# Performance work log

Hardware: AMD Instinct MI355X
Metric: run time of the kernel (lower is better)

Reference implementation:

```python
import jax, jax.numpy as jnp
import numpy as np

DIM = 2048
N_HEADS = 32
HEAD_DIM = DIM // N_HEADS  # 64
ROT_DIM = 32               # partial_rotary_factor = 32/head_dim
ROPE_THETA = 1000000.0
T = 2048
QKV_DIM = 3 * DIM


def setup_inputs() -> dict:
    key = jax.random.key(0)
    ks = jax.random.split(key, 8)
    inp = {
        "positions": jnp.arange(T, dtype=jnp.int32),
        "hidden_states": jax.random.normal(ks[0], (T, DIM), dtype=jnp.float32),
        "Wqkv": jax.random.normal(ks[1], (QKV_DIM, DIM), dtype=jnp.float32) * 0.02,
        "bqkv": jax.random.normal(ks[2], (QKV_DIM,), dtype=jnp.float32) * 0.02,
        "Wout": jax.random.normal(ks[3], (DIM, DIM), dtype=jnp.float32) * 0.02,
        "bout": jax.random.normal(ks[4], (DIM,), dtype=jnp.float32) * 0.02,
        "tau_alpha": jax.random.normal(ks[5], (N_HEADS,), dtype=jnp.float32) * 0.1,
        "tau_wq": jax.random.normal(ks[6], (N_HEADS, QKV_DIM), dtype=jnp.float32) * 0.02,
        "tau_wv": jax.random.normal(ks[7], (N_HEADS, QKV_DIM), dtype=jnp.float32) * 0.02,
    }
    return inp


def _rope_neox(x, positions):
    # x: [T, H, D]; rotate first ROT_DIM dims, neox (half-split) style
    half = ROT_DIM // 2
    inv_freq = 1.0 / (ROPE_THETA ** (jnp.arange(0, ROT_DIM, 2, dtype=jnp.float32) / ROT_DIM))
    ang = positions.astype(jnp.float32)[:, None] * inv_freq[None, :]  # [T, half]
    cos = jnp.cos(ang)[:, None, :]  # [T, 1, half]
    sin = jnp.sin(ang)[:, None, :]
    x1 = x[..., :half]
    x2 = x[..., half:ROT_DIM]
    rot = jnp.concatenate([x1 * cos - x2 * sin, x2 * cos + x1 * sin], axis=-1)
    return jnp.concatenate([rot, x[..., ROT_DIM:]], axis=-1)


def reference(positions, hidden_states, Wqkv, bqkv, Wout, bout, tau_alpha, tau_wq, tau_wv):
    T_, H, D = hidden_states.shape[0], N_HEADS, HEAD_DIM
    qkv = hidden_states @ Wqkv.T + bqkv  # [T, 3*DIM]
    q, k, v = jnp.split(qkv, [DIM, 2 * DIM], axis=-1)

    # tau gating (exact-erf gelu, matching torch F.gelu default)
    tok_feat = jax.nn.gelu(qkv, approximate=False)
    tok_q = jnp.tanh(tok_feat @ tau_wq.T)  # [T, H]
    tok_v = jnp.tanh(tok_feat @ tau_wv.T)
    pos_log = jnp.log(jnp.clip(positions.astype(jnp.float32) + 1.0, 1e-6))  # [T]
    tau_pos = 1.0 + (jax.nn.sigmoid(tau_alpha[None, :] * pos_log[:, None]) - 0.5)  # [T, H]
    tau_q = tok_q + tau_pos
    tau_v = tok_v + tau_pos

    q = q.reshape(T_, H, D) * tau_q[:, :, None]
    k = k.reshape(T_, H, D)
    v = v.reshape(T_, H, D) * tau_v[:, :, None]

    q = _rope_neox(q, positions)
    k = _rope_neox(k, positions)

    # causal attention
    scale = D ** -0.5
    scores = jnp.einsum("thd,shd->hts", q, k) * scale  # [H, T, T]
    causal = positions[:, None] >= positions[None, :]   # [T, T]
    scores = jnp.where(causal[None, :, :], scores, jnp.finfo(scores.dtype).min)
    probs = jax.nn.softmax(scores, axis=-1)
    attn = jnp.einsum("hts,shd->thd", probs, v).reshape(T_, DIM)

    return attn @ Wout.T + bout
```

## Files before the change

kernel.cpp:

```cpp
#include <hip/hip_runtime.h>
#include <math.h>


typedef __bf16 bf16x8 __attribute__((ext_vector_type(8)));
typedef float floatx4 __attribute__((ext_vector_type(4)));
typedef unsigned short ushort8v __attribute__((ext_vector_type(8)));

__device__ __forceinline__ unsigned short f2b(float x) {
    unsigned int b = __float_as_uint(x);
    b = b + 0x7FFFu + ((b >> 16) & 1u);
    return (unsigned short)(b >> 16);
}
__device__ __forceinline__ unsigned short f2b_trunc(float x) {
    return (unsigned short)(__float_as_uint(x) >> 16);
}
__device__ __forceinline__ float b2f(unsigned short u) {
    return __uint_as_float(((unsigned int)u) << 16);
}
__device__ __forceinline__ float gelu_f(float x) {
    return 0.5f * x * (1.0f + erff(x * 0.70710678118654752440f));
}
__device__ __forceinline__ float fexp2(float x) {
    return __builtin_amdgcn_exp2f(x);
}
__device__ __forceinline__ floatx4 mfma16(bf16x8 a, bf16x8 b, floatx4 c) {
    return __builtin_amdgcn_mfma_f32_16x16x32_bf16(a, b, c, 0, 0, 0);
}
__device__ __forceinline__ void gl2lds16(const unsigned short* g, unsigned short* l) {
    __builtin_amdgcn_global_load_lds(
        (__attribute__((address_space(1))) void*)g,
        (__attribute__((address_space(3))) void*)l, 16, 0, 0);
}

__constant__ float INV_FREQ[16] = {
    1.0f, 0.42169650342858224f, 0.17782794100389228f, 0.074989420933245582f,
    0.031622776601683791f, 0.013335214321633240f, 0.0056234132519034908f,
    0.0023713737056616552f, 0.001f, 4.2169650342858224e-4f,
    1.7782794100389228e-4f, 7.4989420933245582e-5f, 3.1622776601683791e-5f,
    1.3335214321633240e-5f, 5.6234132519034908e-6f, 2.3713737056616552e-6f
};

__constant__ unsigned char CHUNK_QT[40] = {
    15,15,15, 14,14,14, 13,13,13, 12,12,12, 11,11, 10,10, 9,9, 8,8, 7,6,5,4,
    15,11,7,3, 14,10,6,2, 13,9,5,1, 12,8,4,0};
__constant__ unsigned char CHUNK_C[40] = {
    0,1,2, 0,1,2, 0,1,2, 0,1,2, 0,1, 0,1, 0,1, 0,1, 0,0,0,0,
    3,2,1,0, 3,2,1,0, 3,2,1,0, 3,2,1,0};

__global__ __launch_bounds__(256) void cvt3_f32_bf16(
    const float* __restrict__ s0, unsigned short* __restrict__ d0, int n0,
    const float* __restrict__ s1, unsigned short* __restrict__ d1, int n1,
    const float* __restrict__ s2, unsigned short* __restrict__ d2, int n2) {
    int i = blockIdx.x * 256 + threadIdx.x;
    const float* s; unsigned short* d;
    if (i < n0)           { s = s0; d = d0; }
    else if (i < n0 + n1) { i -= n0; s = s1; d = d1; }
    else                  { i -= n0 + n1; s = s2; d = d2; if (i >= n2) return; }
    const float4* sp = reinterpret_cast<const float4*>(s) + (size_t)i * 2;
    float4 a = sp[0], b = sp[1];
    ushort8v r;
    r[0] = f2b(a.x); r[1] = f2b(a.y); r[2] = f2b(a.z); r[3] = f2b(a.w);
    r[4] = f2b(b.x); r[5] = f2b(b.y); r[6] = f2b(b.z); r[7] = f2b(b.w);
    *(reinterpret_cast<ushort8v*>(d) + i) = r;
}

__global__ __launch_bounds__(256, 2) void gemm_qkv_p2(
    const unsigned short* __restrict__ A, const unsigned short* __restrict__ B,
    const float* __restrict__ bias, unsigned short* __restrict__ P,
    int M, int N, int K) {
    __shared__ unsigned short Ls[2][20480];
    const int tid = threadIdx.x;
    const int wave = tid >> 6, lane = tid & 63;
    const int row16 = lane & 15, quad = lane >> 4;
    const int wrow = wave >> 1, wcol = wave & 1;
    const int bm0 = blockIdx.y * 128, bn0 = blockIdx.x * 192;
    const int NT = K >> 6;

    floatx4 acc[4][6] = {};

    auto stage_half = [&](int kt, int hf) {
        const bool isB = hf & 1;
        const unsigned short* mat = isB ? B : A;
        const int rbase = isB ? bn0 : bm0;
        const int colb = kt * 64 + (hf >> 1) * 32;
        const int hoff = ((hf & 1) ? 4096 : 0) + (hf >> 1) * 10240;
        unsigned short* dst = &Ls[kt & 1][hoff];
        const int nrd = isB ? 3 : 2;
        #pragma unroll
        for (int rd = 0; rd < 3; ++rd) {
            if (rd >= nrd) break;
            int g = tid + rd * 256;
            int rl = g & 7, c4 = (g >> 3) & 3, r8 = g >> 5;
            gl2lds16(mat + (size_t)(rbase + r8 * 8 + rl) * K + colb + c4 * 8,
                     dst + g * 8);
        }
    };

    stage_half(0, 0); stage_half(0, 1); stage_half(0, 2); stage_half(0, 3);
    stage_half(1, 0); stage_half(1, 1); stage_half(1, 2);
    asm volatile("s_waitcnt vmcnt(7)" ::: "memory");
    __builtin_amdgcn_s_barrier();

    const int ra = wrow * 64 + row16;
    const int rb = wcol * 96 + row16;
    const int aoff = (ra >> 3) * 256 + quad * 64 + (ra & 7) * 8;
    const int boff = (rb >> 3) * 256 + quad * 64 + (rb & 7) * 8;

    for (int kt = 0; kt < NT; ++kt) {
        const int bsel = kt & 1;
        bf16x8 af[4], bfr[3];
        #pragma unroll
        for (int mt = 0; mt < 4; ++mt)
            af[mt] = *reinterpret_cast<const bf16x8*>(&Ls[bsel][aoff + mt * 512]);
        #pragma unroll
        for (int j = 0; j < 3; ++j)
            bfr[j] = *reinterpret_cast<const bf16x8*>(&Ls[bsel][4096 + boff + j * 512]);
        if (kt + 1 < NT) stage_half(kt + 1, 3);
        __builtin_amdgcn_s_barrier();
        asm volatile("s_waitcnt lgkmcnt(0)" ::: "memory");
        __builtin_amdgcn_sched_barrier(0);
        __builtin_amdgcn_s_setprio(1);
        #pragma unroll
        for (int mt = 0; mt < 4; ++mt)
            #pragma unroll
            for (int j = 0; j < 3; ++j)
                acc[mt][j] = mfma16(af[mt], bfr[j], acc[mt][j]);
        __builtin_amdgcn_s_setprio(0);
        __builtin_amdgcn_s_barrier();
        #pragma unroll
        for (int j = 0; j < 3; ++j)
            bfr[j] = *reinterpret_cast<const bf16x8*>(&Ls[bsel][4096 + boff + (3 + j) * 512]);
        if (kt + 2 < NT) stage_half(kt + 2, 0);
        __builtin_amdgcn_s_barrier();
        asm volatile("s_waitcnt lgkmcnt(0)" ::: "memory");
        __builtin_amdgcn_sched_barrier(0);
        __builtin_amdgcn_s_setprio(1);
        #pragma unroll
        for (int mt = 0; mt < 4; ++mt)
            #pragma unroll
            for (int j = 0; j < 3; ++j)
                acc[mt][3 + j] = mfma16(af[mt], bfr[j], acc[mt][3 + j]);
        __builtin_amdgcn_s_setprio(0);
        __builtin_amdgcn_s_barrier();
        #pragma unroll
        for (int mt = 0; mt < 4; ++mt)
            af[mt] = *reinterpret_cast<const bf16x8*>(&Ls[bsel][10240 + aoff + mt * 512]);
        #pragma unroll
        for (int j = 0; j < 3; ++j)
            bfr[j] = *reinterpret_cast<const bf16x8*>(&Ls[bsel][14336 + boff + j * 512]);
        if (kt + 2 < NT) stage_half(kt + 2, 1);
        __builtin_amdgcn_s_barrier();
        asm volatile("s_waitcnt lgkmcnt(0)" ::: "memory");
        __builtin_amdgcn_sched_barrier(0);
        __builtin_amdgcn_s_setprio(1);
        #pragma unroll
        for (int mt = 0; mt < 4; ++mt)
            #pragma unroll
            for (int j = 0; j < 3; ++j)
                acc[mt][j] = mfma16(af[mt], bfr[j], acc[mt][j]);
        __builtin_amdgcn_s_setprio(0);
        __builtin_amdgcn_s_barrier();
        #pragma unroll
        for (int j = 0; j < 3; ++j)
            bfr[j] = *reinterpret_cast<const bf16x8*>(&Ls[bsel][14336 + boff + (3 + j) * 512]);
        if (kt + 2 < NT) stage_half(kt + 2, 2);
        if (kt == NT - 2)     asm volatile("s_waitcnt vmcnt(0)" ::: "memory");
        else if (kt < NT - 2) asm volatile("s_waitcnt vmcnt(7)" ::: "memory");
        __builtin_amdgcn_s_barrier();
        asm volatile("s_waitcnt lgkmcnt(0)" ::: "memory");
        __builtin_amdgcn_sched_barrier(0);
        __builtin_amdgcn_s_setprio(1);
        #pragma unroll
        for (int mt = 0; mt < 4; ++mt)
            #pragma unroll
            for (int j = 0; j < 3; ++j)
                acc[mt][3 + j] = mfma16(af[mt], bfr[j], acc[mt][3 + j]);
        __builtin_amdgcn_s_setprio(0);
        __builtin_amdgcn_s_barrier();
    }

    #pragma unroll
    for (int mt = 0; mt < 4; ++mt) {
        #pragma unroll
        for (int nt = 0; nt < 6; ++nt) {
            int gc = bn0 + wcol * 96 + nt * 16 + row16;
            float bv = bias[gc];
            int gr0 = bm0 + wrow * 64 + mt * 16 + quad * 4;
            #pragma unroll
            for (int i = 0; i < 4; ++i)
                P[(size_t)(gr0 + i) * N + gc] = f2b(acc[mt][nt][i] + bv);
        }
    }
}

template <int BM, int BN, bool OUT_BF16>
__global__ __launch_bounds__(256) void gemm_bf16_bt(
    const unsigned short* __restrict__ A, const unsigned short* __restrict__ B,
    const float* __restrict__ bias, void* __restrict__ Cout,
    int M, int N, int K) {
    constexpr int MT = BM / 32, NT = BN / 32;
    __shared__ unsigned short As[BM * 64];
    __shared__ unsigned short Bs[BN * 64];
    const int tid = threadIdx.x;
    const int wave = tid >> 6, lane = tid & 63;
    const int row16 = lane & 15, quad = lane >> 4;
    const int wm = (wave >> 1) * (BM / 2), wn = (wave & 1) * (BN / 2);
    const int bm0 = blockIdx.y * BM, bn0 = blockIdx.x * BN;
    const int rl = lane & 7, cl = lane >> 3;

    floatx4 acc[MT][NT] = {};

    for (int k0 = 0; k0 < K; k0 += 64) {
        __syncthreads();
        #pragma unroll
        for (int j = 0; j < BM / 32; ++j) {
            int unit = wave * (BM / 32) + j;
            const unsigned short* ga = A + (size_t)(bm0 + unit * 8 + rl) * K + k0 + cl * 8;
            gl2lds16(ga, &As[unit * 512 + lane * 8]);
        }
        #pragma unroll
        for (int j = 0; j < BN / 32; ++j) {
            int unit = wave * (BN / 32) + j;
            const unsigned short* gb = B + (size_t)(bn0 + unit * 8 + rl) * K + k0 + cl * 8;
            gl2lds16(gb, &Bs[unit * 512 + lane * 8]);
        }
        __syncthreads();

        #pragma unroll
        for (int ks = 0; ks < 2; ++ks) {
            bf16x8 af[MT], bfr[NT];
            #pragma unroll
            for (int mt = 0; mt < MT; ++mt) {
                int r = wm + mt * 16 + row16;
                af[mt] = *reinterpret_cast<const bf16x8*>(
                    &As[(r >> 3) * 512 + (ks * 4 + quad) * 64 + (r & 7) * 8]);
            }
            #pragma unroll
            for (int nt = 0; nt < NT; ++nt) {
                int r = wn + nt * 16 + row16;
                bfr[nt] = *reinterpret_cast<const bf16x8*>(
                    &Bs[(r >> 3) * 512 + (ks * 4 + quad) * 64 + (r & 7) * 8]);
            }
            #pragma unroll
            for (int mt = 0; mt < MT; ++mt)
                #pragma unroll
                for (int nt = 0; nt < NT; ++nt)
                    acc[mt][nt] = mfma16(af[mt], bfr[nt], acc[mt][nt]);
        }
    }

    #pragma unroll
    for (int mt = 0; mt < MT; ++mt) {
        #pragma unroll
        for (int nt = 0; nt < NT; ++nt) {
            int gc = bn0 + wn + nt * 16 + row16;
            float bv = bias[gc];
            int gr0 = bm0 + wm + mt * 16 + quad * 4;
            #pragma unroll
            for (int i = 0; i < 4; ++i) {
                float v = acc[mt][nt][i] + bv;
                if (OUT_BF16)
                    ((unsigned short*)Cout)[(size_t)(gr0 + i) * N + gc] = f2b(v);
                else
                    ((float*)Cout)[(size_t)(gr0 + i) * N + gc] = v;
            }
        }
    }
}

template <int KSPLIT>
__global__ __launch_bounds__(256) void tok_gemm_splitk(
    const unsigned short* __restrict__ A0,
    const float* __restrict__ Bq, const float* __restrict__ Bv,
    float* __restrict__ C, int K) {
    constexpr int LDT = 72;
    __shared__ unsigned short As[64 * LDT];
    __shared__ unsigned short Bs[64 * LDT];
    const int tid = threadIdx.x;
    const int wave = tid >> 6, lane = tid & 63;
    const int row16 = lane & 15, quad = lane >> 4;
    const int wm = (wave >> 1) * 32, wn = (wave & 1) * 32;
    const int bm0 = blockIdx.y * 64;
    const int kbeg = blockIdx.x * KSPLIT;

    floatx4 acc[2][2] = {};

    for (int k0 = kbeg; k0 < kbeg + KSPLIT; k0 += 64) {
        #pragma unroll
        for (int it = 0; it < 2; ++it) {
            int i = tid + it * 256;
            int r = i >> 3, c8 = i & 7;
            size_t off = (size_t)(bm0 + r) * K + k0 + c8 * 8;
            ushort8v a0 = *reinterpret_cast<const ushort8v*>(A0 + off);
            ushort8v g;
            #pragma unroll
            for (int j = 0; j < 8; ++j) g[j] = f2b(gelu_f(b2f(a0[j])));
            *reinterpret_cast<ushort8v*>(&As[r * LDT + c8 * 8]) = g;

            const float* brow = (r < 32) ? (Bq + (size_t)r * K) : (Bv + (size_t)(r - 32) * K);
            float4 w0 = *reinterpret_cast<const float4*>(brow + k0 + c8 * 8);
            float4 w1 = *reinterpret_cast<const float4*>(brow + k0 + c8 * 8 + 4);
            ushort8v wb;
            wb[0] = f2b(w0.x); wb[1] = f2b(w0.y); wb[2] = f2b(w0.z); wb[3] = f2b(w0.w);
            wb[4] = f2b(w1.x); wb[5] = f2b(w1.y); wb[6] = f2b(w1.z); wb[7] = f2b(w1.w);
            *reinterpret_cast<ushort8v*>(&Bs[r * LDT + c8 * 8]) = wb;
        }
        __syncthreads();

        #pragma unroll
        for (int ks = 0; ks < 2; ++ks) {
            bf16x8 af[2], bfr[2];
            #pragma unroll
            for (int mt = 0; mt < 2; ++mt)
                af[mt] = *reinterpret_cast<const bf16x8*>(
                    &As[(wm + mt * 16 + row16) * LDT + ks * 32 + quad * 8]);
            #pragma unroll
            for (int nt = 0; nt < 2; ++nt)
                bfr[nt] = *reinterpret_cast<const bf16x8*>(
                    &Bs[(wn + nt * 16 + row16) * LDT + ks * 32 + quad * 8]);
            #pragma unroll
            for (int mt = 0; mt < 2; ++mt)
                #pragma unroll
                for (int nt = 0; nt < 2; ++nt)
                    acc[mt][nt] = mfma16(af[mt], bfr[nt], acc[mt][nt]);
        }
        __syncthreads();
    }

    #pragma unroll
    for (int mt = 0; mt < 2; ++mt)
        #pragma unroll
        for (int nt = 0; nt < 2; ++nt) {
            int gc = wn + nt * 16 + row16;
            int gr0 = bm0 + wm + mt * 16 + quad * 4;
            #pragma unroll
            for (int i = 0; i < 4; ++i)
                atomicAdd(&C[(size_t)(gr0 + i) * 64 + gc], acc[mt][nt][i]);
        }
}

__global__ __launch_bounds__(256) void qkv_process(
    const unsigned short* __restrict__ P,
    const float* __restrict__ tok_raw, const float* __restrict__ tau_alpha,
    const int* __restrict__ positions, unsigned short* __restrict__ qh,
    unsigned short* __restrict__ kh, unsigned short* __restrict__ vpk) {
    const int h = blockIdx.y;
    const int t0 = blockIdx.x * 64;
    const int tid = threadIdx.x;
    __shared__ float vtr[64][65];
    __shared__ float tauq_s[64], tauv_s[64];

    if (tid < 64) {
        int t = t0 + tid;
        float pos = (float)positions[t];
        float pl = logf(fmaxf(pos + 1.0f, 1e-6f));
        float a = tau_alpha[h];
        float tp = 0.5f + 1.0f / (1.0f + __expf(-a * pl));
        tauq_s[tid] = tanhf(tok_raw[t * 64 + h]) + tp;
        tauv_s[tid] = tanhf(tok_raw[t * 64 + 32 + h]) + tp;
    }
    __syncthreads();

    const float QSCALE = 0.18033688011112042f;
    #pragma unroll
    for (int it = 0; it < 2; ++it) {
        int idx = tid + it * 256;
        int tl = idx >> 3, c8 = idx & 7;
        int t = t0 + tl;
        size_t rb = (size_t)t * 6144 + h * 64 + c8 * 8;
        ushort8v q0v = *reinterpret_cast<const ushort8v*>(P + rb);
        ushort8v k0v = *reinterpret_cast<const ushort8v*>(P + rb + 2048);
        ushort8v v0v = *reinterpret_cast<const ushort8v*>(P + rb + 4096);
        float tq = tauq_s[tl], tv = tauv_s[tl];
        float qo[8], ko[8];
        #pragma unroll
        for (int j = 0; j < 8; ++j) {
            qo[j] = b2f(q0v[j]) * tq;
            ko[j] = b2f(k0v[j]);
        }
        if (c8 < 4) {
            size_t rp = (size_t)t * 6144 + h * 64 + (c8 ^ 2) * 8;
            ushort8v qp0 = *reinterpret_cast<const ushort8v*>(P + rp);
            ushort8v kp0 = *reinterpret_cast<const ushort8v*>(P + rp + 2048);
            float pos = (float)positions[t];
            float sgn = (c8 < 2) ? -1.0f : 1.0f;
            #pragma unroll
            for (int j = 0; j < 8; ++j) {
                int fi = (c8 * 8 + j) & 15;
                float ang = pos * INV_FREQ[fi];
                float s, c;
                sincosf(ang, &s, &c);
                float qp = b2f(qp0[j]) * tq;
                float kp = b2f(kp0[j]);
                qo[j] = qo[j] * c + sgn * qp * s;
                ko[j] = ko[j] * c + sgn * kp * s;
            }
        }
        size_t ob = ((size_t)h * 2048 + t) * 64 + c8 * 8;
        ushort8v qw, kw;
        #pragma unroll
        for (int j = 0; j < 8; ++j) {
            qw[j] = f2b(qo[j] * QSCALE);
            kw[j] = f2b(ko[j]);
        }
        *reinterpret_cast<ushort8v*>(qh + ob) = qw;
        *reinterpret_cast<ushort8v*>(kh + ob) = kw;
        #pragma unroll
        for (int j = 0; j < 8; ++j)
            vtr[c8 * 8 + j][tl] = b2f(v0v[j]) * tv;
    }
    __syncthreads();
    #pragma unroll
    for (int it = 0; it < 2; ++it) {
        int idx = tid + it * 256;
        int d = idx >> 3, tc = (idx & 7) * 8;
        int sb = (t0 + tc) >> 5;
        int quad = (tc & 31) >> 3;
        int nt = d >> 4, m = d & 15;
        ushort8v w;
        #pragma unroll
        for (int j = 0; j < 8; ++j) w[j] = f2b(vtr[d][tc + j]);
        *reinterpret_cast<ushort8v*>(
            vpk + (size_t)h * 131072 + sb * 2048 + nt * 512 + quad * 128 + m * 8) = w;
    }
}

__global__ __launch_bounds__(256) void attn_fa(
    const unsigned short* __restrict__ qh, const unsigned short* __restrict__ kh,
    const unsigned short* __restrict__ vpk, unsigned short* __restrict__ Opart,
    float* __restrict__ ml) {
    constexpr int LD = 72;
    __shared__ unsigned short pbuf[4][2][16 * LD];
    const int b = blockIdx.x;
    const int h = (b & 7) + 8 * ((b >> 3) & 3);
    const int cpos = b >> 5;
    const int qt = CHUNK_QT[cpos], ch = CHUNK_C[cpos];
    const int q0 = qt * 128;
    const int slot = (h * 16 + qt) * 4 + ch;
    const int wave = threadIdx.x >> 6, lane = threadIdx.x & 63;
    const int m = lane & 15, quad = lane >> 4;
    const int qrow0 = q0 + wave * 32;
    const int sbeg = ch * 512;
    const int send = min(sbeg + 512, qrow0 + 32);

    bf16x8 aq[2][2];
    #pragma unroll
    for (int mt = 0; mt < 2; ++mt) {
        const unsigned short* qptr = qh + ((size_t)h * 2048 + qrow0 + mt * 16 + m) * 64;
        aq[mt][0] = *reinterpret_cast<const bf16x8*>(qptr + quad * 8);
        aq[mt][1] = *reinterpret_cast<const bf16x8*>(qptr + 32 + quad * 8);
    }
    const unsigned short* kbase = kh + (size_t)h * 2048 * 64;
    const unsigned short* vbase = vpk + (size_t)h * 131072;

    floatx4 o[2][4] = {};
    float lsum[2][4] = {};

    for (int s0 = sbeg; s0 < send; s0 += 64) {
        floatx4 sc[2][4];
        #pragma unroll
        for (int sg = 0; sg < 4; ++sg) {
            const unsigned short* kr = kbase + (size_t)(s0 + sg * 16 + m) * 64;
            bf16x8 bk0 = *reinterpret_cast<const bf16x8*>(kr + quad * 8);
            bf16x8 bk1 = *reinterpret_cast<const bf16x8*>(kr + 32 + quad * 8);
            #pragma unroll
            for (int mt = 0; mt < 2; ++mt) {
                floatx4 z = {};
                z = mfma16(aq[mt][0], bk0, z);
                z = mfma16(aq[mt][1], bk1, z);
                sc[mt][sg] = z;
            }
        }
        if (s0 + 63 > qrow0) {
            #pragma unroll
            for (int mt = 0; mt < 2; ++mt)
                #pragma unroll
                for (int sg = 0; sg < 4; ++sg)
                    #pragma unroll
                    for (int i = 0; i < 4; ++i) {
                        int t = qrow0 + mt * 16 + quad * 4 + i;
                        int s = s0 + sg * 16 + m;
                        sc[mt][sg][i] = (s > t) ? -1e30f : sc[mt][sg][i];
                    }
        }
        #pragma unroll
        for (int mt = 0; mt < 2; ++mt)
            #pragma unroll
            for (int sg = 0; sg < 4; ++sg)
                #pragma unroll
                for (int i = 0; i < 4; ++i)
                    sc[mt][sg][i] = fexp2(sc[mt][sg][i]);
        #pragma unroll
        for (int mt = 0; mt < 2; ++mt)
            #pragma unroll
            for (int i = 0; i < 4; ++i)
                lsum[mt][i] += (sc[mt][0][i] + sc[mt][1][i]) + (sc[mt][2][i] + sc[mt][3][i]);

        unsigned short* pb0 = pbuf[wave][0];
        unsigned short* pb1 = pbuf[wave][1];
        #pragma unroll
        for (int sg = 0; sg < 4; ++sg)
            #pragma unroll
            for (int i = 0; i < 4; ++i) {
                pb0[(quad * 4 + i) * LD + sg * 16 + m] = f2b_trunc(sc[0][sg][i]);
                pb1[(quad * 4 + i) * LD + sg * 16 + m] = f2b_trunc(sc[1][sg][i]);
            }
        bf16x8 ap[2][2];
        #pragma unroll
        for (int mt = 0; mt < 2; ++mt) {
            ap[mt][0] = *reinterpret_cast<const bf16x8*>(&pbuf[wave][mt][m * LD + quad * 8]);
            ap[mt][1] = *reinterpret_cast<const bf16x8*>(&pbuf[wave][mt][m * LD + 32 + quad * 8]);
        }
        #pragma unroll
        for (int c = 0; c < 2; ++c) {
            const unsigned short* vrow = vbase + ((s0 >> 5) + c) * 2048;
            #pragma unroll
            for (int nt = 0; nt < 4; ++nt) {
                bf16x8 bv = *reinterpret_cast<const bf16x8*>(vrow + nt * 512 + lane * 8);
                o[0][nt] = mfma16(ap[0][c], bv, o[0][nt]);
                o[1][nt] = mfma16(ap[1][c], bv, o[1][nt]);
            }
        }
    }

    #pragma unroll
    for (int d = 1; d < 16; d <<= 1)
        #pragma unroll
        for (int mt = 0; mt < 2; ++mt)
            #pragma unroll
            for (int i = 0; i < 4; ++i)
                lsum[mt][i] += __shfl_xor(lsum[mt][i], d, 16);
    #pragma unroll
    for (int mt = 0; mt < 2; ++mt) {
        #pragma unroll
        for (int nt = 0; nt < 4; ++nt)
            #pragma unroll
            for (int i = 0; i < 4; ++i)
                Opart[((size_t)slot * 128 + wave * 32 + mt * 16 + quad * 4 + i) * 64 + nt * 16 + m]
                    = f2b(o[mt][nt][i]);
        if (m == 0) {
            #pragma unroll
            for (int i = 0; i < 4; ++i)
                ml[(size_t)slot * 128 + wave * 32 + mt * 16 + quad * 4 + i] = lsum[mt][i];
        }
    }
}

__global__ __launch_bounds__(256) void attn_merge(
    const unsigned short* __restrict__ Opart, const float* __restrict__ ml,
    unsigned short* __restrict__ attnb) {
    const int qt = blockIdx.x, h = blockIdx.y;
    const int nc = qt / 4 + 1;
    const int tid = threadIdx.x;
    const int r = tid >> 1, dh = (tid & 1) * 32;
    const int bs = (h * 16 + qt) * 4;

    float denom = 0.0f;
    #pragma unroll
    for (int c = 0; c < 4; ++c)
        if (c < nc) denom += ml[(size_t)(bs + c) * 128 + r];
    float inv = 1.0f / denom;

    float acc[32] = {};
    #pragma unroll
    for (int c = 0; c < 4; ++c) {
        if (c < nc) {
            const unsigned short* op = Opart + ((size_t)(bs + c) * 128 + r) * 64 + dh;
            #pragma unroll
            for (int j = 0; j < 4; ++j) {
                ushort8v v = *reinterpret_cast<const ushort8v*>(op + j * 8);
                #pragma unroll
                for (int k = 0; k < 8; ++k)
                    acc[j * 8 + k] += b2f(v[k]);
            }
        }
    }
    unsigned short* dst = attnb + (size_t)(qt * 128 + r) * 2048 + h * 64 + dh;
    #pragma unroll
    for (int j = 0; j < 4; ++j) {
        ushort8v v;
        #pragma unroll
        for (int k = 0; k < 8; ++k) v[k] = f2b(acc[j * 8 + k] * inv);
        *reinterpret_cast<ushort8v*>(dst + j * 8) = v;
    }
}

extern "C" void kernel_launch(void* const* d_in, const int* in_sizes, int n_in,
                              void* d_out, int out_size, void* d_ws, size_t ws_size,
                              hipStream_t stream) {
    const int*   positions = (const int*)d_in[0];
    const float* hidden    = (const float*)d_in[1];
    const float* Wqkv      = (const float*)d_in[2];
    const float* bqkv      = (const float*)d_in[3];
    const float* Wout      = (const float*)d_in[4];
    const float* bout      = (const float*)d_in[5];
    const float* tau_alpha = (const float*)d_in[6];
    const float* tau_wq    = (const float*)d_in[7];
    const float* tau_wv    = (const float*)d_in[8];

    unsigned char* ws = (unsigned char*)d_ws;
    unsigned short* P       = (unsigned short*)(ws);
    unsigned short* Opart   = (unsigned short*)(ws);
    unsigned short* wqb     = (unsigned short*)(ws + 50331648);
    unsigned short* qh      = (unsigned short*)(ws + 50331648);
    unsigned short* kh      = (unsigned short*)(ws + 58720256);
    unsigned short* vpk     = (unsigned short*)(ws + 67108864);
    unsigned short* hb      = (unsigned short*)(ws + 75497472);
    float*          tok_raw = (float*)(ws + 75497472);
    unsigned short* attnb   = (unsigned short*)(ws + 75497472);
    float*          ml      = (float*)(ws + 83886080);
    unsigned short* wob     = (unsigned short*)(ws + 85983232);

    cvt3_f32_bf16<<<10240, 256, 0, stream>>>(
        hidden, hb, 524288, Wqkv, wqb, 1572864, Wout, wob, 524288);
    gemm_qkv_p2<<<dim3(32, 16), 256, 0, stream>>>(
        hb, wqb, bqkv, P, 2048, 6144, 2048);
    hipMemsetAsync(tok_raw, 0, (size_t)2048 * 64 * 4, stream);
    tok_gemm_splitk<256><<<dim3(24, 32), 256, 0, stream>>>(
        P, tau_wq, tau_wv, tok_raw, 6144);
    qkv_process<<<dim3(32, 32), 256, 0, stream>>>(
        P, tok_raw, tau_alpha, positions, qh, kh, vpk);
    attn_fa<<<1280, 256, 0, stream>>>(qh, kh, vpk, Opart, ml);
    attn_merge<<<dim3(16, 32), 256, 0, stream>>>(Opart, ml, attnb);
    gemm_bf16_bt<64, 64, false><<<dim3(32, 32), 256, 0, stream>>>(
        attnb, wob, bout, d_out, 2048, 2048, 2048);
}
```

Measured before the change: 382.0 us.

## Enlarge QKV GEMM tile to 256x192 with 8 waves and fewer LDS reloads

```diff
diff --git a/kernel.cpp b/kernel.cpp
--- a/kernel.cpp
+++ b/kernel.cpp
@@ -64,57 +64,70 @@
     *(reinterpret_cast<ushort8v*>(d) + i) = r;
 }
 
-__global__ __launch_bounds__(256, 2) void gemm_qkv_p2(
+__global__ __launch_bounds__(512, 1) void gemm_qkv_fg(
     const unsigned short* __restrict__ A, const unsigned short* __restrict__ B,
     const float* __restrict__ bias, unsigned short* __restrict__ P,
     int M, int N, int K) {
-    __shared__ unsigned short Ls[2][20480];
+    __shared__ unsigned short Ls[2][28672];
     const int tid = threadIdx.x;
     const int wave = tid >> 6, lane = tid & 63;
     const int row16 = lane & 15, quad = lane >> 4;
-    const int wrow = wave >> 1, wcol = wave & 1;
-    const int bm0 = blockIdx.y * 128, bn0 = blockIdx.x * 192;
+    const int wrow = wave >> 2, wcol = wave & 3;
+    const int bm0 = blockIdx.y * 256, bn0 = blockIdx.x * 192;
     const int NT = K >> 6;
 
-    floatx4 acc[4][6] = {};
+    floatx4 acc[8][3] = {};
 
     auto stage_half = [&](int kt, int hf) {
         const bool isB = hf & 1;
         const unsigned short* mat = isB ? B : A;
         const int rbase = isB ? bn0 : bm0;
         const int colb = kt * 64 + (hf >> 1) * 32;
-        const int hoff = ((hf & 1) ? 4096 : 0) + (hf >> 1) * 10240;
-        unsigned short* dst = &Ls[kt & 1][hoff];
-        const int nrd = isB ? 3 : 2;
-        #pragma unroll
-        for (int rd = 0; rd < 3; ++rd) {
-            if (rd >= nrd) break;
-            int g = tid + rd * 256;
-            int rl = g & 7, c4 = (g >> 3) & 3, r8 = g >> 5;
-            gl2lds16(mat + (size_t)(rbase + r8 * 8 + rl) * K + colb + c4 * 8,
-                     dst + g * 8);
+        unsigned short* dst = &Ls[kt & 1][(hf >> 1) * 14336 + (isB ? 8192 : 0)];
+        if (isB) {
+            {
+                int g = tid;
+                int rl = g & 7, c4 = (g >> 3) & 3, r8 = g >> 5;
+                gl2lds16(mat + (size_t)(rbase + r8 * 8 + rl) * K + colb + c4 * 8,
+                         dst + g * 8);
+            }
+            if (tid < 256) {
+                int g = 512 + tid;
+                int rl = g & 7, c4 = (g >> 3) & 3, r8 = g >> 5;
+                gl2lds16(mat + (size_t)(rbase + r8 * 8 + rl) * K + colb + c4 * 8,
+                         dst + g * 8);
+            }
+        } else {
+            #pragma unroll
+            for (int rd = 0; rd < 2; ++rd) {
+                int g = tid + rd * 512;
+                int rl = g & 7, c4 = (g >> 3) & 3, r8 = g >> 5;
+                gl2lds16(mat + (size_t)(rbase + r8 * 8 + rl) * K + colb + c4 * 8,
+                         dst + g * 8);
+            }
         }
     };
 
     stage_half(0, 0); stage_half(0, 1); stage_half(0, 2); stage_half(0, 3);
     stage_half(1, 0); stage_half(1, 1); stage_half(1, 2);
-    asm volatile("s_waitcnt vmcnt(7)" ::: "memory");
+    if (wave < 4) asm volatile("s_waitcnt vmcnt(6)" ::: "memory");
+    else          asm volatile("s_waitcnt vmcnt(5)" ::: "memory");
     __builtin_amdgcn_s_barrier();
 
-    const int ra = wrow * 64 + row16;
-    const int rb = wcol * 96 + row16;
+    const int ra = wrow * 128 + row16;
+    const int rb = wcol * 48 + row16;
     const int aoff = (ra >> 3) * 256 + quad * 64 + (ra & 7) * 8;
     const int boff = (rb >> 3) * 256 + quad * 64 + (rb & 7) * 8;
 
     for (int kt = 0; kt < NT; ++kt) {
         const int bsel = kt & 1;
-        bf16x8 af[4], bfr[3];
-        #pragma unroll
-        for (int mt = 0; mt < 4; ++mt)
+        bf16x8 af[8], bfr[3];
+        #pragma unroll
+        for (int mt = 0; mt < 8; ++mt)
             af[mt] = *reinterpret_cast<const bf16x8*>(&Ls[bsel][aoff + mt * 512]);
         #pragma unroll
         for (int j = 0; j < 3; ++j)
-            bfr[j] = *reinterpret_cast<const bf16x8*>(&Ls[bsel][4096 + boff + j * 512]);
+            bfr[j] = *reinterpret_cast<const bf16x8*>(&Ls[bsel][8192 + boff + j * 512]);
         if (kt + 1 < NT) stage_half(kt + 1, 3);
         __builtin_amdgcn_s_barrier();
         asm volatile("s_waitcnt lgkmcnt(0)" ::: "memory");
@@ -127,27 +140,22 @@
                 acc[mt][j] = mfma16(af[mt], bfr[j], acc[mt][j]);
         __builtin_amdgcn_s_setprio(0);
         __builtin_amdgcn_s_barrier();
-        #pragma unroll
-        for (int j = 0; j < 3; ++j)
-            bfr[j] = *reinterpret_cast<const bf16x8*>(&Ls[bsel][4096 + boff + (3 + j) * 512]);
         if (kt + 2 < NT) stage_half(kt + 2, 0);
-        __builtin_amdgcn_s_barrier();
-        asm volatile("s_waitcnt lgkmcnt(0)" ::: "memory");
         __builtin_amdgcn_sched_barrier(0);
         __builtin_amdgcn_s_setprio(1);
         #pragma unroll
         for (int mt = 0; mt < 4; ++mt)
             #pragma unroll
             for (int j = 0; j < 3; ++j)
-                acc[mt][3 + j] = mfma16(af[mt], bfr[j], acc[mt][3 + j]);
+                acc[4 + mt][j] = mfma16(af[4 + mt], bfr[j], acc[4 + mt][j]);
         __builtin_amdgcn_s_setprio(0);
         __builtin_amdgcn_s_barrier();
         #pragma unroll
-        for (int mt = 0; mt < 4; ++mt)
-            af[mt] = *reinterpret_cast<const bf16x8*>(&Ls[bsel][10240 + aoff + mt * 512]);
+        for (int mt = 0; mt < 8; ++mt)
+            af[mt] = *reinterpret_cast<const bf16x8*>(&Ls[bsel][14336 + aoff + mt * 512]);
         #pragma unroll
         for (int j = 0; j < 3; ++j)
-            bfr[j] = *reinterpret_cast<const bf16x8*>(&Ls[bsel][14336 + boff + j * 512]);
+            bfr[j] = *reinterpret_cast<const bf16x8*>(&Ls[bsel][22528 + boff + j * 512]);
         if (kt + 2 < NT) stage_half(kt + 2, 1);
         __builtin_amdgcn_s_barrier();
         asm volatile("s_waitcnt lgkmcnt(0)" ::: "memory");
@@ -160,32 +168,31 @@
                 acc[mt][j] = mfma16(af[mt], bfr[j], acc[mt][j]);
         __builtin_amdgcn_s_setprio(0);
         __builtin_amdgcn_s_barrier();
-        #pragma unroll
-        for (int j = 0; j < 3; ++j)
-            bfr[j] = *reinterpret_cast<const bf16x8*>(&Ls[bsel][14336 + boff + (3 + j) * 512]);
         if (kt + 2 < NT) stage_half(kt + 2, 2);
-        if (kt == NT - 2)     asm volatile("s_waitcnt vmcnt(0)" ::: "memory");
-        else if (kt < NT - 2) asm volatile("s_waitcnt vmcnt(7)" ::: "memory");
-        __builtin_amdgcn_s_barrier();
-        asm volatile("s_waitcnt lgkmcnt(0)" ::: "memory");
+        if (kt == NT - 2) {
+            asm volatile("s_waitcnt vmcnt(0)" ::: "memory");
+        } else if (kt < NT - 2) {
+            if (wave < 4) asm volatile("s_waitcnt vmcnt(6)" ::: "memory");
+            else          asm volatile("s_waitcnt vmcnt(5)" ::: "memory");
+        }
         __builtin_amdgcn_sched_barrier(0);
         __builtin_amdgcn_s_setprio(1);
         #pragma unroll
         for (int mt = 0; mt < 4; ++mt)
             #pragma unroll
             for (int j = 0; j < 3; ++j)
-                acc[mt][3 + j] = mfma16(af[mt], bfr[j], acc[mt][3 + j]);
+                acc[4 + mt][j] = mfma16(af[4 + mt], bfr[j], acc[4 + mt][j]);
         __builtin_amdgcn_s_setprio(0);
         __builtin_amdgcn_s_barrier();
     }
 
     #pragma unroll
-    for (int mt = 0; mt < 4; ++mt) {
-        #pragma unroll
-        for (int nt = 0; nt < 6; ++nt) {
-            int gc = bn0 + wcol * 96 + nt * 16 + row16;
+    for (int mt = 0; mt < 8; ++mt) {
+        #pragma unroll
+        for (int nt = 0; nt < 3; ++nt) {
+            int gc = bn0 + wcol * 48 + nt * 16 + row16;
             float bv = bias[gc];
-            int gr0 = bm0 + wrow * 64 + mt * 16 + quad * 4;
+            int gr0 = bm0 + wrow * 128 + mt * 16 + quad * 4;
             #pragma unroll
             for (int i = 0; i < 4; ++i)
                 P[(size_t)(gr0 + i) * N + gc] = f2b(acc[mt][nt][i] + bv);
@@ -613,7 +620,7 @@
 
     cvt3_f32_bf16<<<10240, 256, 0, stream>>>(
         hidden, hb, 524288, Wqkv, wqb, 1572864, Wout, wob, 524288);
-    gemm_qkv_p2<<<dim3(32, 16), 256, 0, stream>>>(
+    gemm_qkv_fg<<<dim3(32, 8), 512, 0, stream>>>(
         hb, wqb, bqkv, P, 2048, 6144, 2048);
     hipMemsetAsync(tok_raw, 0, (size_t)2048 * 64 * 4, stream);
     tok_gemm_splitk<256><<<dim3(24, 32), 256, 0, stream>>>(
```

Measured after the change: 367.7 us. -3.7%, faster.
